# Optimization experiments

Measured on AMD Instinct MI355X. Metric: run time of the kernel, lower is better.

The kernel has to match this reference:

```python
import jax, jax.numpy as jnp
import numpy as np

BN_EPS = 1e-5


def setup_inputs() -> dict:
    key = jax.random.key(0)
    ks = jax.random.split(key, 12)
    B, N, G, D = 16, 8192, 64, 384
    C_IN = D + 64 + 3  # 451
    inp = {
        "features": jax.random.normal(ks[0], (B, G, D), jnp.float32),
        "centers": jax.random.normal(ks[1], (B, G, 3), jnp.float32),
        "pc": jax.random.normal(ks[2], (B, N, 3), jnp.float32),
        "category": jax.random.randint(ks[3], (B,), 0, 16, jnp.int64),
        "cat_embed": jax.random.normal(ks[4], (16, 64), jnp.float32) * 0.02,
        "w1": jax.random.normal(ks[5], (256, C_IN), jnp.float32) * (1.0 / np.sqrt(C_IN)),
        "b1": jnp.zeros((256,), jnp.float32),
        "g1": jnp.ones((256,), jnp.float32),
        "be1": jnp.zeros((256,), jnp.float32),
        "m1": jnp.zeros((256,), jnp.float32),
        "v1": jnp.ones((256,), jnp.float32),
        "w2": jax.random.normal(ks[6], (256, 256), jnp.float32) * (1.0 / 16.0),
        "b2": jnp.zeros((256,), jnp.float32),
        "g2": jnp.ones((256,), jnp.float32),
        "be2": jnp.zeros((256,), jnp.float32),
        "m2": jnp.zeros((256,), jnp.float32),
        "v2": jnp.ones((256,), jnp.float32),
        "w3": jax.random.normal(ks[7], (50, 256), jnp.float32) * (1.0 / 16.0),
        "b3": jnp.zeros((50,), jnp.float32),
    }
    return inp


def _bn(x, g, be, m, v):  # x: [B, N, C], inference-mode BatchNorm1d
    return (x - m) * (g * jax.lax.rsqrt(v + BN_EPS)) + be


def reference(features, centers, pc, category, cat_embed,
              w1, b1, g1, be1, m1, v1,
              w2, b2, g2, be2, m2, v2,
              w3, b3):
    B, N, _ = pc.shape
    # Euclidean cdist via norm expansion: [B, N, G]
    p2 = jnp.sum(pc * pc, axis=-1, keepdims=True)            # [B,N,1]
    c2 = jnp.sum(centers * centers, axis=-1)[:, None, :]     # [B,1,G]
    dot = jnp.einsum('bnd,bgd->bng', pc, centers)
    dist = jnp.sqrt(jnp.clip(p2 + c2 - 2.0 * dot, 1e-12))
    # top-3 smallest
    neg_d, knn_idx = jax.lax.top_k(-dist, 3)                 # [B,N,3]
    knn_dist = -neg_d
    w = 1.0 / (knn_dist + 1e-8)
    w = w / jnp.sum(w, axis=-1, keepdims=True)               # [B,N,3]
    # gather per-batch: features [B,G,D], knn_idx [B,N,3] -> [B,N,3,D]
    knn_features = jax.vmap(lambda f, i: f[i])(features, knn_idx)
    point_features = jnp.einsum('bnkd,bnk->bnd', knn_features, w)  # [B,N,D]
    cat_feat = jnp.broadcast_to(cat_embed[category][:, None, :], (B, N, 64))
    combined = jnp.concatenate([point_features, cat_feat, pc], axis=-1)  # [B,N,451]
    # Conv1d(k=1) == per-point dense layer; keep [B,N,C] layout
    h = jnp.einsum('bnc,oc->bno', combined, w1) + b1
    h = jax.nn.relu(_bn(h, g1, be1, m1, v1))
    h = jnp.einsum('bnc,oc->bno', h, w2) + b2
    h = jax.nn.relu(_bn(h, g2, be2, m2, v2))
    seg_logits = jnp.einsum('bnc,oc->bno', h, w3) + b3       # [B,N,50]
    return seg_logits
```

## Files before the change

kernel.cpp:

```cpp
#include <hip/hip_runtime.h>

typedef unsigned short u16;
typedef unsigned int u32;
typedef short short8 __attribute__((ext_vector_type(8)));
typedef float f32x4 __attribute__((ext_vector_type(4)));

#define KEEP(x) asm volatile("" :: "v"(x))
#define BN_EPS 1e-5f

__device__ __forceinline__ u16 f2bf(float x) {
  union { float f; u32 u; } v;
  v.f = x;
  u32 r = v.u + 0x7FFFu + ((v.u >> 16) & 1u);
  return (u16)(r >> 16);
}

__global__ __launch_bounds__(256, 2)
void gcalc_all(const float* __restrict__ features, const int* __restrict__ category,
               const float* __restrict__ cat_embed,
               const float* __restrict__ w1, const float* __restrict__ b1,
               const float* __restrict__ g1, const float* __restrict__ be1,
               const float* __restrict__ m1, const float* __restrict__ v1,
               const float* __restrict__ w2, const float* __restrict__ g2,
               const float* __restrict__ b2, const float* __restrict__ be2,
               const float* __restrict__ m2, const float* __restrict__ v2,
               const float* __restrict__ w3,
               u16* __restrict__ G, float* __restrict__ bias1,
               u16* __restrict__ w2b, u16* __restrict__ w3b, float* __restrict__ b2p)
{
  __shared__ u16 Fs[64 * 392];
  const int bid = blockIdx.x;
  const int tid = threadIdx.x;

  if (bid < 64) {
    const int b    = bid >> 2;
    const int och0 = (bid & 3) * 64;
    const int lane = tid & 63;
    const int wv   = tid >> 6;
    const int lr   = lane & 15;
    const int lk   = (lane >> 4) * 8;
    const int r0   = (lane >> 4) * 4;

    const f32x4* F4 = (const f32x4*)(features + b * 24576);
    #pragma unroll
    for (int it = 0; it < 24; ++it) {
      int idx = tid + 256 * it;
      int c = idx / 96;
      int d4 = idx - c * 96;
      f32x4 v = F4[c * 96 + d4];
      u32 lo = (u32)f2bf(v[0]) | ((u32)f2bf(v[1]) << 16);
      u32 hi = (u32)f2bf(v[2]) | ((u32)f2bf(v[3]) << 16);
      *(uint2*)&Fs[c * 392 + d4 * 4] = make_uint2(lo, hi);
    }

    if (tid < 64) {
      int o = och0 + tid;
      float s1 = g1[o] * rsqrtf(v1[o] + BN_EPS);
      float acc = (b1[o] - m1[o]) * s1 + be1[o];
      const float* wr = w1 + o * 451 + 384;
      const float* ce = cat_embed + category[b] * 64;
      #pragma unroll 8
      for (int j = 0; j < 64; ++j) acc += wr[j] * s1 * ce[j];
      bias1[b * 256 + o] = acc;
      u16* Go = G + (b * 256 + o) * 96;
      Go[64] = f2bf(wr[64] * s1);
      Go[65] = f2bf(wr[65] * s1);
      Go[66] = f2bf(wr[66] * s1);
      #pragma unroll
      for (int k = 67; k < 96; ++k) Go[k] = 0;
    }
    __syncthreads();

    const int ch = och0 + wv * 16 + lr;
    const float s1 = g1[ch] * rsqrtf(v1[ch] + BN_EPS);
    f32x4 acc[4];
    {
      f32x4 z = {0.f, 0.f, 0.f, 0.f};
      #pragma unroll
      for (int m = 0; m < 4; ++m) acc[m] = z;
    }
    #pragma unroll
    for (int ks = 0; ks < 12; ++ks) {
      const float* wr = w1 + ch * 451 + ks * 32 + lk;
      short8 bv;
      #pragma unroll
      for (int e = 0; e < 8; ++e) bv[e] = (short)f2bf(wr[e] * s1);
      #pragma unroll
      for (int m = 0; m < 4; ++m) {
        short8 av = *(const short8*)(&Fs[(m * 16 + lr) * 392 + ks * 32 + lk]);
        acc[m] = __builtin_amdgcn_mfma_f32_16x16x32_bf16(av, bv, acc[m], 0, 0, 0);
      }
    }
    #pragma unroll
    for (int m = 0; m < 4; ++m)
      #pragma unroll
      for (int r = 0; r < 4; ++r)
        G[(b * 256 + ch) * 96 + m * 16 + r0 + r] = f2bf(acc[m][r]);

  } else if (bid < 80) {
    int base = (bid - 64) * 4096;
    #pragma unroll
    for (int e = 0; e < 16; ++e) {
      int i = base + e * 256 + tid;
      int o = i >> 8;
      float s2 = g2[o] * rsqrtf(v2[o] + BN_EPS);
      w2b[i] = f2bf(w2[i] * s2);
    }
  } else {
    #pragma unroll
    for (int e = 0; e < 64; ++e) {
      int i = e * 256 + tid;
      int o = i >> 8;
      w3b[i] = (o < 50) ? f2bf(w3[i]) : (u16)0;
    }
    {
      float s2 = g2[tid] * rsqrtf(v2[tid] + BN_EPS);
      b2p[tid] = (b2[tid] - m2[tid]) * s2 + be2[tid];
    }
  }
}

#define LDP 104
#define LDH 264

__global__ __launch_bounds__(512, 4)
void fused_kernel(const float* __restrict__ centers, const float* __restrict__ pc,
                  const u16* __restrict__ G, const float* __restrict__ bias1,
                  const u16* __restrict__ w2b, const u16* __restrict__ w3b,
                  const float* __restrict__ b2p, const float* __restrict__ b3,
                  float* __restrict__ out)
{
  __shared__ u16 hbuf[128 * LDH];
  __shared__ float centl[192];
  __shared__ float pcl[384];

  const int bx   = ((blockIdx.x & 7) << 7) | (blockIdx.x >> 3);
  const int b    = bx >> 6;
  const int n0   = (bx & 63) << 7;
  const int tid  = threadIdx.x;
  const int lane = tid & 63;
  const int wv   = tid >> 6;
  const int lr   = lane & 15;
  const int lk   = (lane >> 4) * 8;
  const int r0   = (lane >> 4) * 4;

  u16*   Pm   = hbuf;
  float* scrd = (float*)((char*)hbuf + 32768);
  int*   scri = (int*)((char*)hbuf + 40960);

  short8 bvG[3][2];
  #pragma unroll
  for (int ks = 0; ks < 3; ++ks)
    #pragma unroll
    for (int n = 0; n < 2; ++n)
      bvG[ks][n] = *(const short8*)(G + (b * 256 + wv * 32 + n * 16 + lr) * 96 + ks * 32 + lk);

  {
    u32* Pw = (u32*)Pm;
    #pragma unroll
    for (int i = 0; i < 13; ++i) Pw[tid + 512 * i] = 0;
  }
  if (tid < 192) centl[tid] = centers[b * 192 + tid];
  if (tid < 384) pcl[tid] = pc[(b * 8192 + n0) * 3 + tid];
  __syncthreads();

  {
    int p = tid >> 2, c = tid & 3;
    float px = pcl[p * 3 + 0], py = pcl[p * 3 + 1], pz = pcl[p * 3 + 2];
    float p2 = px * px + py * py + pz * pz;
    float bd0 = 3.4e38f, bd1 = 3.4e38f, bd2 = 3.4e38f;
    int bi0 = 0, bi1 = 0, bi2 = 0;
    int j0 = c * 16;
    for (int j = j0; j < j0 + 16; ++j) {
      float cx = centl[j * 3 + 0], cy = centl[j * 3 + 1], cz = centl[j * 3 + 2];
      float dotv = px * cx + py * cy + pz * cz;
      float c2 = cx * cx + cy * cy + cz * cz;
      float d2 = (p2 + c2) - 2.f * dotv;
      if (d2 < bd2) {
        if (d2 < bd1) {
          if (d2 < bd0) { bd2 = bd1; bi2 = bi1; bd1 = bd0; bi1 = bi0; bd0 = d2; bi0 = j; }
          else          { bd2 = bd1; bi2 = bi1; bd1 = d2; bi1 = j; }
        } else          { bd2 = d2; bi2 = j; }
      }
    }
    scrd[tid * 3 + 0] = bd0; scrd[tid * 3 + 1] = bd1; scrd[tid * 3 + 2] = bd2;
    scri[tid * 3 + 0] = bi0; scri[tid * 3 + 1] = bi1; scri[tid * 3 + 2] = bi2;
  }
  __syncthreads();

  if (tid < 128) {
    float bd0 = 3.4e38f, bd1 = 3.4e38f, bd2 = 3.4e38f;
    int bi0 = 0, bi1 = 0, bi2 = 0;
    #pragma unroll
    for (int c = 0; c < 4; ++c) {
      int t = tid * 4 + c;
      #pragma unroll
      for (int s = 0; s < 3; ++s) {
        float d2 = scrd[t * 3 + s];
        int   j  = scri[t * 3 + s];
        if (d2 < bd2) {
          if (d2 < bd1) {
            if (d2 < bd0) { bd2 = bd1; bi2 = bi1; bd1 = bd0; bi1 = bi0; bd0 = d2; bi0 = j; }
            else          { bd2 = bd1; bi2 = bi1; bd1 = d2; bi1 = j; }
          } else          { bd2 = d2; bi2 = j; }
        }
      }
    }
    float dd0 = sqrtf(fmaxf(bd0, 1e-12f));
    float dd1 = sqrtf(fmaxf(bd1, 1e-12f));
    float dd2 = sqrtf(fmaxf(bd2, 1e-12f));
    float u0 = 1.f / (dd0 + 1e-8f);
    float u1 = 1.f / (dd1 + 1e-8f);
    float u2 = 1.f / (dd2 + 1e-8f);
    float inv = 1.f / (u0 + u1 + u2);
    u16* Pr = Pm + tid * LDP;
    Pr[bi0] = f2bf(u0 * inv);
    Pr[bi1] = f2bf(u1 * inv);
    Pr[bi2] = f2bf(u2 * inv);
    Pr[64] = f2bf(pcl[tid * 3 + 0]);
    Pr[65] = f2bf(pcl[tid * 3 + 1]);
    Pr[66] = f2bf(pcl[tid * 3 + 2]);
  }
  KEEP(bvG[0][0]); KEEP(bvG[0][1]); KEEP(bvG[1][0]);
  KEEP(bvG[1][1]); KEEP(bvG[2][0]); KEEP(bvG[2][1]);
  __syncthreads();

  f32x4 acc[8][2];
  {
    f32x4 z = {0.f, 0.f, 0.f, 0.f};
    #pragma unroll
    for (int m = 0; m < 8; ++m) { acc[m][0] = z; acc[m][1] = z; }
  }
  #pragma unroll
  for (int ks = 0; ks < 3; ++ks) {
    short8 av[8];
    #pragma unroll
    for (int m = 0; m < 8; ++m)
      av[m] = *(const short8*)(&Pm[(m * 16 + lr) * LDP + ks * 32 + lk]);
    #pragma unroll
    for (int m = 0; m < 8; ++m)
      #pragma unroll
      for (int n = 0; n < 2; ++n)
        acc[m][n] = __builtin_amdgcn_mfma_f32_16x16x32_bf16(av[m], bvG[ks][n], acc[m][n], 0, 0, 0);
  }
  __syncthreads();

  #pragma unroll
  for (int n = 0; n < 2; ++n) {
    float bb = bias1[b * 256 + wv * 32 + n * 16 + lr];
    #pragma unroll
    for (int m = 0; m < 8; ++m)
      #pragma unroll
      for (int r = 0; r < 4; ++r) {
        float v = acc[m][n][r] + bb;
        v = v > 0.f ? v : 0.f;
        int row = m * 16 + r0 + r;
        int col = (wv * 32 + n * 16 + lr) ^ (((row >> 2) & 7) << 3);
        hbuf[row * LDH + col] = f2bf(v);
      }
  }
  __syncthreads();

  {
    f32x4 z = {0.f, 0.f, 0.f, 0.f};
    #pragma unroll
    for (int m = 0; m < 8; ++m) { acc[m][0] = z; acc[m][1] = z; }
  }
  #pragma unroll
  for (int ks = 0; ks < 8; ++ks) {
    short8 bv[2];
    #pragma unroll
    for (int n = 0; n < 2; ++n)
      bv[n] = *(const short8*)(w2b + (wv * 32 + n * 16 + lr) * 256 + ks * 32 + lk);
    short8 av[8];
    #pragma unroll
    for (int m = 0; m < 8; ++m) {
      int row = m * 16 + lr;
      int g = (ks * 4 + (lane >> 4)) ^ ((row >> 2) & 7);
      av[m] = *(const short8*)(&hbuf[row * LDH + g * 8]);
    }
    #pragma unroll
    for (int m = 0; m < 8; ++m)
      #pragma unroll
      for (int n = 0; n < 2; ++n)
        acc[m][n] = __builtin_amdgcn_mfma_f32_16x16x32_bf16(av[m], bv[n], acc[m][n], 0, 0, 0);
  }
  __syncthreads();

  #pragma unroll
  for (int n = 0; n < 2; ++n) {
    float bb = b2p[wv * 32 + n * 16 + lr];
    #pragma unroll
    for (int m = 0; m < 8; ++m)
      #pragma unroll
      for (int r = 0; r < 4; ++r) {
        float v = acc[m][n][r] + bb;
        v = v > 0.f ? v : 0.f;
        int row = m * 16 + r0 + r;
        int col = (wv * 32 + n * 16 + lr) ^ (((row >> 2) & 7) << 3);
        hbuf[row * LDH + col] = f2bf(v);
      }
  }

  const int wm = wv & 3;
  const int wn = wv >> 2;
  short8 w3f[8][2];
  #pragma unroll
  for (int ks = 0; ks < 8; ++ks)
    #pragma unroll
    for (int j = 0; j < 2; ++j)
      w3f[ks][j] = *(const short8*)(w3b + (wn * 32 + j * 16 + lr) * 256 + ks * 32 + lk);
  #pragma unroll
  for (int ks = 0; ks < 8; ++ks) { KEEP(w3f[ks][0]); KEEP(w3f[ks][1]); }
  __syncthreads();

  {
    f32x4 acc3[2][2];
    f32x4 z = {0.f, 0.f, 0.f, 0.f};
    acc3[0][0] = z; acc3[0][1] = z; acc3[1][0] = z; acc3[1][1] = z;
    #pragma unroll
    for (int ks = 0; ks < 8; ++ks) {
      #pragma unroll
      for (int mi = 0; mi < 2; ++mi) {
        int row = (wm * 2 + mi) * 16 + lr;
        int g = (ks * 4 + (lane >> 4)) ^ ((row >> 2) & 7);
        short8 av = *(const short8*)(&hbuf[row * LDH + g * 8]);
        #pragma unroll
        for (int j = 0; j < 2; ++j)
          acc3[mi][j] = __builtin_amdgcn_mfma_f32_16x16x32_bf16(av, w3f[ks][j], acc3[mi][j], 0, 0, 0);
      }
    }
    #pragma unroll
    for (int j = 0; j < 2; ++j) {
      int c = wn * 32 + j * 16 + lr;
      if (c < 50) {
        float b3v = b3[c];
        #pragma unroll
        for (int mi = 0; mi < 2; ++mi)
          #pragma unroll
          for (int r = 0; r < 4; ++r) {
            int row = n0 + (wm * 2 + mi) * 16 + r0 + r;
            out[(b * 8192 + row) * 50 + c] = acc3[mi][j][r] + b3v;
          }
      }
    }
  }
}

extern "C" void kernel_launch(void* const* d_in, const int* in_sizes, int n_in,
                              void* d_out, int out_size, void* d_ws, size_t ws_size,
                              hipStream_t stream) {
  const float* features  = (const float*)d_in[0];
  const float* centers   = (const float*)d_in[1];
  const float* pc        = (const float*)d_in[2];
  const int*   category  = (const int*)d_in[3];
  const float* cat_embed = (const float*)d_in[4];
  const float* w1  = (const float*)d_in[5];
  const float* b1  = (const float*)d_in[6];
  const float* g1  = (const float*)d_in[7];
  const float* be1 = (const float*)d_in[8];
  const float* m1  = (const float*)d_in[9];
  const float* v1  = (const float*)d_in[10];
  const float* w2  = (const float*)d_in[11];
  const float* b2  = (const float*)d_in[12];
  const float* g2  = (const float*)d_in[13];
  const float* be2 = (const float*)d_in[14];
  const float* m2  = (const float*)d_in[15];
  const float* v2  = (const float*)d_in[16];
  const float* w3  = (const float*)d_in[17];
  const float* b3  = (const float*)d_in[18];
  float* out = (float*)d_out;

  char* ws = (char*)d_ws;
  u16*   w2b   = (u16*)(ws);
  u16*   w3b   = (u16*)(ws + 131072);
  float* b2p   = (float*)(ws + 163840);
  u16*   G     = (u16*)(ws + 164864);
  float* bias1 = (float*)(ws + 951296);

  gcalc_all<<<81, 256, 0, stream>>>(features, category, cat_embed,
                                    w1, b1, g1, be1, m1, v1,
                                    w2, g2, b2, be2, m2, v2, w3,
                                    G, bias1, w2b, w3b, b2p);

  fused_kernel<<<1024, 512, 0, stream>>>(centers, pc, G, bias1,
                                         w2b, w3b, b2p, b3, out);
}
```

Before: 169.4 us.

## Shuffle-based top-3 merge, prefetch W2 slices, coalesce final output via LDS staging

```diff
diff --git a/kernel.cpp b/kernel.cpp
--- a/kernel.cpp
+++ b/kernel.cpp
@@ -144,9 +144,7 @@
   const int lk   = (lane >> 4) * 8;
   const int r0   = (lane >> 4) * 4;
 
-  u16*   Pm   = hbuf;
-  float* scrd = (float*)((char*)hbuf + 32768);
-  int*   scri = (int*)((char*)hbuf + 40960);
+  u16* Pm = hbuf;
 
   short8 bvG[3][2];
   #pragma unroll
@@ -165,12 +163,12 @@
   __syncthreads();
 
   {
-    int p = tid >> 2, c = tid & 3;
+    int p = tid >> 2, c4 = tid & 3;
     float px = pcl[p * 3 + 0], py = pcl[p * 3 + 1], pz = pcl[p * 3 + 2];
     float p2 = px * px + py * py + pz * pz;
     float bd0 = 3.4e38f, bd1 = 3.4e38f, bd2 = 3.4e38f;
     int bi0 = 0, bi1 = 0, bi2 = 0;
-    int j0 = c * 16;
+    int j0 = c4 * 16;
     for (int j = j0; j < j0 + 16; ++j) {
       float cx = centl[j * 3 + 0], cy = centl[j * 3 + 1], cz = centl[j * 3 + 2];
       float dotv = px * cx + py * cy + pz * cz;
@@ -183,43 +181,40 @@
         } else          { bd2 = d2; bi2 = j; }
       }
     }
-    scrd[tid * 3 + 0] = bd0; scrd[tid * 3 + 1] = bd1; scrd[tid * 3 + 2] = bd2;
-    scri[tid * 3 + 0] = bi0; scri[tid * 3 + 1] = bi1; scri[tid * 3 + 2] = bi2;
-  }
-  __syncthreads();
-
-  if (tid < 128) {
-    float bd0 = 3.4e38f, bd1 = 3.4e38f, bd2 = 3.4e38f;
-    int bi0 = 0, bi1 = 0, bi2 = 0;
+    float md0 = 3.4e38f, md1 = 3.4e38f, md2 = 3.4e38f;
+    int mi0 = 0, mi1 = 0, mi2 = 0;
+    auto INS = [&](float d, int j) {
+      if (d < md2) {
+        if (d < md1) {
+          if (d < md0) { md2 = md1; mi2 = mi1; md1 = md0; mi1 = mi0; md0 = d; mi0 = j; }
+          else         { md2 = md1; mi2 = mi1; md1 = d; mi1 = j; }
+        } else         { md2 = d; mi2 = j; }
+      }
+    };
+    int gl = lane & ~3;
     #pragma unroll
     for (int c = 0; c < 4; ++c) {
-      int t = tid * 4 + c;
-      #pragma unroll
-      for (int s = 0; s < 3; ++s) {
-        float d2 = scrd[t * 3 + s];
-        int   j  = scri[t * 3 + s];
-        if (d2 < bd2) {
-          if (d2 < bd1) {
-            if (d2 < bd0) { bd2 = bd1; bi2 = bi1; bd1 = bd0; bi1 = bi0; bd0 = d2; bi0 = j; }
-            else          { bd2 = bd1; bi2 = bi1; bd1 = d2; bi1 = j; }
-          } else          { bd2 = d2; bi2 = j; }
-        }
-      }
-    }
-    float dd0 = sqrtf(fmaxf(bd0, 1e-12f));
-    float dd1 = sqrtf(fmaxf(bd1, 1e-12f));
-    float dd2 = sqrtf(fmaxf(bd2, 1e-12f));
-    float u0 = 1.f / (dd0 + 1e-8f);
-    float u1 = 1.f / (dd1 + 1e-8f);
-    float u2 = 1.f / (dd2 + 1e-8f);
-    float inv = 1.f / (u0 + u1 + u2);
-    u16* Pr = Pm + tid * LDP;
-    Pr[bi0] = f2bf(u0 * inv);
-    Pr[bi1] = f2bf(u1 * inv);
-    Pr[bi2] = f2bf(u2 * inv);
-    Pr[64] = f2bf(pcl[tid * 3 + 0]);
-    Pr[65] = f2bf(pcl[tid * 3 + 1]);
-    Pr[66] = f2bf(pcl[tid * 3 + 2]);
+      int src = gl + c;
+      float d0 = __shfl(bd0, src), d1 = __shfl(bd1, src), d2 = __shfl(bd2, src);
+      int   e0 = __shfl(bi0, src), e1 = __shfl(bi1, src), e2 = __shfl(bi2, src);
+      INS(d0, e0); INS(d1, e1); INS(d2, e2);
+    }
+    if (c4 == 0) {
+      float dd0 = sqrtf(fmaxf(md0, 1e-12f));
+      float dd1 = sqrtf(fmaxf(md1, 1e-12f));
+      float dd2 = sqrtf(fmaxf(md2, 1e-12f));
+      float u0 = 1.f / (dd0 + 1e-8f);
+      float u1 = 1.f / (dd1 + 1e-8f);
+      float u2 = 1.f / (dd2 + 1e-8f);
+      float inv = 1.f / (u0 + u1 + u2);
+      u16* Pr = Pm + p * LDP;
+      Pr[mi0] = f2bf(u0 * inv);
+      Pr[mi1] = f2bf(u1 * inv);
+      Pr[mi2] = f2bf(u2 * inv);
+      Pr[64] = f2bf(px);
+      Pr[65] = f2bf(py);
+      Pr[66] = f2bf(pz);
+    }
   }
   KEEP(bvG[0][0]); KEEP(bvG[0][1]); KEEP(bvG[1][0]);
   KEEP(bvG[1][1]); KEEP(bvG[2][0]); KEEP(bvG[2][1]);
@@ -244,6 +239,13 @@
         acc[m][n] = __builtin_amdgcn_mfma_f32_16x16x32_bf16(av[m], bvG[ks][n], acc[m][n], 0, 0, 0);
   }
   __syncthreads();
+
+  short8 w2f[4][2];
+  #pragma unroll
+  for (int ks = 0; ks < 4; ++ks)
+    #pragma unroll
+    for (int n = 0; n < 2; ++n)
+      w2f[ks][n] = *(const short8*)(w2b + (wv * 32 + n * 16 + lr) * 256 + ks * 32 + lk);
 
   #pragma unroll
   for (int n = 0; n < 2; ++n) {
@@ -259,6 +261,8 @@
         hbuf[row * LDH + col] = f2bf(v);
       }
   }
+  KEEP(w2f[0][0]); KEEP(w2f[0][1]); KEEP(w2f[1][0]); KEEP(w2f[1][1]);
+  KEEP(w2f[2][0]); KEEP(w2f[2][1]); KEEP(w2f[3][0]); KEEP(w2f[3][1]);
   __syncthreads();
 
   {
@@ -269,9 +273,12 @@
   #pragma unroll
   for (int ks = 0; ks < 8; ++ks) {
     short8 bv[2];
-    #pragma unroll
-    for (int n = 0; n < 2; ++n)
-      bv[n] = *(const short8*)(w2b + (wv * 32 + n * 16 + lr) * 256 + ks * 32 + lk);
+    if (ks < 4) { bv[0] = w2f[ks][0]; bv[1] = w2f[ks][1]; }
+    else {
+      #pragma unroll
+      for (int n = 0; n < 2; ++n)
+        bv[n] = *(const short8*)(w2b + (wv * 32 + n * 16 + lr) * 256 + ks * 32 + lk);
+    }
     short8 av[8];
     #pragma unroll
     for (int m = 0; m < 8; ++m) {
@@ -301,47 +308,45 @@
         hbuf[row * LDH + col] = f2bf(v);
       }
   }
-
-  const int wm = wv & 3;
-  const int wn = wv >> 2;
-  short8 w3f[8][2];
-  #pragma unroll
-  for (int ks = 0; ks < 8; ++ks)
-    #pragma unroll
-    for (int j = 0; j < 2; ++j)
-      w3f[ks][j] = *(const short8*)(w3b + (wn * 32 + j * 16 + lr) * 256 + ks * 32 + lk);
-  #pragma unroll
-  for (int ks = 0; ks < 8; ++ks) { KEEP(w3f[ks][0]); KEEP(w3f[ks][1]); }
-  __syncthreads();
-
-  {
-    f32x4 acc3[2][2];
-    f32x4 z = {0.f, 0.f, 0.f, 0.f};
-    acc3[0][0] = z; acc3[0][1] = z; acc3[1][0] = z; acc3[1][1] = z;
+  __syncthreads();
+
+  {
+    f32x4 acc3[4];
+    {
+      f32x4 z = {0.f, 0.f, 0.f, 0.f};
+      #pragma unroll
+      for (int n = 0; n < 4; ++n) acc3[n] = z;
+    }
+    const int row = wv * 16 + lr;
     #pragma unroll
     for (int ks = 0; ks < 8; ++ks) {
-      #pragma unroll
-      for (int mi = 0; mi < 2; ++mi) {
-        int row = (wm * 2 + mi) * 16 + lr;
-        int g = (ks * 4 + (lane >> 4)) ^ ((row >> 2) & 7);
-        short8 av = *(const short8*)(&hbuf[row * LDH + g * 8]);
-        #pragma unroll
-        for (int j = 0; j < 2; ++j)
-          acc3[mi][j] = __builtin_amdgcn_mfma_f32_16x16x32_bf16(av, w3f[ks][j], acc3[mi][j], 0, 0, 0);
-      }
-    }
-    #pragma unroll
-    for (int j = 0; j < 2; ++j) {
-      int c = wn * 32 + j * 16 + lr;
+      int g = (ks * 4 + (lane >> 4)) ^ ((row >> 2) & 7);
+      short8 av = *(const short8*)(&hbuf[row * LDH + g * 8]);
+      #pragma unroll
+      for (int n = 0; n < 4; ++n) {
+        short8 bv = *(const short8*)(w3b + (n * 16 + lr) * 256 + ks * 32 + lk);
+        acc3[n] = __builtin_amdgcn_mfma_f32_16x16x32_bf16(av, bv, acc3[n], 0, 0, 0);
+      }
+    }
+    float* patch = (float*)(hbuf + wv * 16 * LDH);
+    #pragma unroll
+    for (int n = 0; n < 4; ++n) {
+      int c = n * 16 + lr;
       if (c < 50) {
         float b3v = b3[c];
         #pragma unroll
-        for (int mi = 0; mi < 2; ++mi)
-          #pragma unroll
-          for (int r = 0; r < 4; ++r) {
-            int row = n0 + (wm * 2 + mi) * 16 + r0 + r;
-            out[(b * 8192 + row) * 50 + c] = acc3[mi][j][r] + b3v;
-          }
+        for (int r = 0; r < 4; ++r)
+          patch[(r0 + r) * 52 + c] = acc3[n][r] + b3v;
+      }
+    }
+    float* outb = out + (size_t)(b * 8192 + n0 + wv * 16) * 50;
+    #pragma unroll
+    for (int it = 0; it < 13; ++it) {
+      int f = it * 64 + lane;
+      if (f < 800) {
+        int rr = (f * 5243) >> 18;
+        int cc = f - rr * 50;
+        outb[f] = patch[rr * 52 + cc];
       }
     }
   }
```

Result: slower. 187.4 us (+10.6%).
